# Kernel optimization log

Hardware: AMD Instinct MI355X
Metric: run time of the kernel (lower is better)

## Reference

```python
import jax, jax.numpy as jnp
import numpy as np

B, H, W, C = 64, 224, 224, 3
K = 16          # num_clusters
ITERS = 10      # num_iterations
N = H * W       # pixels per image


def _kmeans_single(x, key):
    # x: [N, D] pixels of one image
    # random shuffle -> first K rows as initial centroids (matches tf.random.shuffle + slice)
    perm = jax.random.permutation(key, N)
    cent0 = x[perm[:K]]  # [K, D]

    def step(cent, _):
        # pairwise squared distances: [K, N]
        d = jnp.sum(jnp.square(x[None, :, :] - cent[:, None, :]), axis=2)
        assign = jnp.argmin(d, axis=0)                      # [N] int
        onehot = jax.nn.one_hot(assign, K, dtype=x.dtype)   # [N, K]
        sums = onehot.T @ x                                 # [K, D]
        counts = jnp.sum(onehot, axis=0)[:, None]           # [K, 1]
        # mean of assigned pixels; empty cluster -> 0/0 = NaN, same as tf.reduce_mean of empty
        new_cent = sums / counts
        return new_cent, None

    cent, _ = jax.lax.scan(step, cent0, None, length=ITERS)
    return cent.reshape(K * C)  # tf.reshape(centroids, [dims*num_clusters]) on [K,D]


def setup_inputs() -> dict:
    key = jax.random.key(0)
    inputs = jax.random.uniform(key, (B, H, W, C), dtype=jnp.float32) * 255.0
    return {"inputs": inputs}


def reference(inputs):
    x = inputs.astype(jnp.float32).reshape(B, N, C)
    keys = jax.random.split(jax.random.key(42), B)
    return jax.vmap(_kmeans_single)(x, keys)  # [B, K*C]
```

## Files before the change

kernel.cpp:

```cpp
#include <hip/hip_runtime.h>
#include <stdint.h>


#define NB    64
#define NPIX  50176
#define NK    16
#define NCH   3
#define NITER 10
#define HBINS 2048
#define CANDCAP 1024
#define COLLCAP 128
#define NBLK  512
#define NGRP  8
#define GRPSZ (NBLK / NGRP)
#define CHUNK (NPIX / 8)
#define NQUADS (CHUNK / 4)

typedef unsigned long long u64;

struct KeyPair { uint32_t a, b; };

__device__ __forceinline__ uint32_t rotl32(uint32_t v, uint32_t r) {
  return (v << r) | (v >> (32u - r));
}
__device__ __forceinline__ void tf_round(uint32_t& x0, uint32_t& x1, uint32_t r) {
  x0 += x1; x1 = rotl32(x1, r); x1 ^= x0;
}

__device__ __forceinline__ KeyPair threefry(uint32_t k0, uint32_t k1,
                                            uint32_t x0, uint32_t x1) {
  const uint32_t ks2 = k0 ^ k1 ^ 0x1BD11BDAu;
  x0 += k0; x1 += k1;
  tf_round(x0, x1, 13u); tf_round(x0, x1, 15u); tf_round(x0, x1, 26u); tf_round(x0, x1, 6u);
  x0 += k1;  x1 += ks2 + 1u;
  tf_round(x0, x1, 17u); tf_round(x0, x1, 29u); tf_round(x0, x1, 16u); tf_round(x0, x1, 24u);
  x0 += ks2; x1 += k0 + 2u;
  tf_round(x0, x1, 13u); tf_round(x0, x1, 15u); tf_round(x0, x1, 26u); tf_round(x0, x1, 6u);
  x0 += k0;  x1 += k1 + 3u;
  tf_round(x0, x1, 17u); tf_round(x0, x1, 29u); tf_round(x0, x1, 16u); tf_round(x0, x1, 24u);
  x0 += k1;  x1 += ks2 + 4u;
  tf_round(x0, x1, 13u); tf_round(x0, x1, 15u); tf_round(x0, x1, 26u); tf_round(x0, x1, 6u);
  x0 += ks2; x1 += k0 + 5u;
  KeyPair r; r.a = x0; r.b = x1; return r;
}

__device__ __forceinline__ uint32_t sortkey(KeyPair S, uint32_t i) {
  KeyPair r = threefry(S.a, S.b, 0u, i);
  return r.a ^ r.b;
}

__device__ __forceinline__ void derive_keys(int b, KeyPair& S1, KeyPair& S2) {
  KeyPair root; root.a = 0u; root.b = 42u;
  KeyPair kb = threefry(root.a, root.b, 0u, (uint32_t)b);
  KeyPair K1 = threefry(kb.a, kb.b, 0u, 0u);
  S1 = threefry(kb.a, kb.b, 0u, 1u);
  S2 = threefry(K1.a, K1.b, 0u, 1u);
}

#define T2VAL 27394240u

__device__ __forceinline__ uint32_t ald_u32(const uint32_t* p) {
  return __hip_atomic_load(p, __ATOMIC_RELAXED, __HIP_MEMORY_SCOPE_AGENT);
}
__device__ __forceinline__ void ast_f64(double* p, double v) {
  __hip_atomic_store(p, v, __ATOMIC_RELAXED, __HIP_MEMORY_SCOPE_AGENT);
}
__device__ __forceinline__ double ald_f64(const double* p) {
  return __hip_atomic_load(p, __ATOMIC_RELAXED, __HIP_MEMORY_SCOPE_AGENT);
}


__device__ __forceinline__ void gbar_full(uint32_t* bar, int blk) {
  __syncthreads();
  if (threadIdx.x == 0) {
    uint32_t* grp  = bar + ((blk & (NGRP - 1)) << 4);
    uint32_t* root = bar + 128;
    uint32_t* gen  = bar + 144;
    uint32_t g = __hip_atomic_load(gen, __ATOMIC_RELAXED, __HIP_MEMORY_SCOPE_AGENT);
    __builtin_amdgcn_fence(__ATOMIC_RELEASE, "agent");
    uint32_t a = __hip_atomic_fetch_add(grp, 1u, __ATOMIC_RELAXED,
                                        __HIP_MEMORY_SCOPE_AGENT);
    if (a == (uint32_t)GRPSZ - 1u) {
      __hip_atomic_store(grp, 0u, __ATOMIC_RELAXED, __HIP_MEMORY_SCOPE_AGENT);
      uint32_t r = __hip_atomic_fetch_add(root, 1u, __ATOMIC_RELAXED,
                                          __HIP_MEMORY_SCOPE_AGENT);
      if (r == (uint32_t)NGRP - 1u) {
        __hip_atomic_store(root, 0u, __ATOMIC_RELAXED, __HIP_MEMORY_SCOPE_AGENT);
        __hip_atomic_store(gen, g + 1u, __ATOMIC_RELEASE, __HIP_MEMORY_SCOPE_AGENT);
      } else {
        while (__hip_atomic_load(gen, __ATOMIC_RELAXED,
                                 __HIP_MEMORY_SCOPE_AGENT) == g)
          __builtin_amdgcn_s_sleep(1);
      }
    } else {
      while (__hip_atomic_load(gen, __ATOMIC_RELAXED,
                               __HIP_MEMORY_SCOPE_AGENT) == g)
        __builtin_amdgcn_s_sleep(1);
    }
    __builtin_amdgcn_fence(__ATOMIC_ACQUIRE, "agent");
  }
  __syncthreads();
}

__device__ __forceinline__ void gbar_light(uint32_t* bar, int blk) {
  __syncthreads();
  if (threadIdx.x == 0) {
    uint32_t* grp  = bar + ((blk & (NGRP - 1)) << 4);
    uint32_t* root = bar + 128;
    uint32_t* gen  = bar + 144;
    uint32_t g = __hip_atomic_load(gen, __ATOMIC_RELAXED, __HIP_MEMORY_SCOPE_AGENT);
    uint32_t a = __hip_atomic_fetch_add(grp, 1u, __ATOMIC_RELEASE,
                                        __HIP_MEMORY_SCOPE_AGENT);
    if (a == (uint32_t)GRPSZ - 1u) {
      uint32_t r = __hip_atomic_fetch_add(root, 1u, __ATOMIC_RELEASE,
                                          __HIP_MEMORY_SCOPE_AGENT);
      if (r == (uint32_t)NGRP - 1u) {
        __hip_atomic_store(root, 0u, __ATOMIC_RELAXED, __HIP_MEMORY_SCOPE_AGENT);
        __hip_atomic_store(grp, 0u, __ATOMIC_RELAXED, __HIP_MEMORY_SCOPE_AGENT);
        __hip_atomic_fetch_add(gen, 1u, __ATOMIC_RELAXED, __HIP_MEMORY_SCOPE_AGENT);
      } else {
        __hip_atomic_store(grp, 0u, __ATOMIC_RELAXED, __HIP_MEMORY_SCOPE_AGENT);
        while (__hip_atomic_load(gen, __ATOMIC_RELAXED,
                                 __HIP_MEMORY_SCOPE_AGENT) == g)
          __builtin_amdgcn_s_sleep(1);
      }
    } else {
      while (__hip_atomic_load(gen, __ATOMIC_RELAXED,
                               __HIP_MEMORY_SCOPE_AGENT) == g)
        __builtin_amdgcn_s_sleep(1);
    }
  }
  __syncthreads();
}

union SMem {
  struct { uint32_t lh[HBINS]; } p1;
  struct { u64 sc[CANDCAP]; uint32_t sh[HBINS]; uint32_t S[HBINS];
           uint32_t ts[256]; uint32_t Rt[NK]; } p2;
  struct { uint32_t bs[NK]; } p3;
  struct { u64 lc[NK * COLLCAP]; int jsel[NK]; } p4;
  struct { float accf[64 * 256]; } p5;
};

__global__ __launch_bounds__(256, 2) void mega(
    const float* __restrict__ x, float* __restrict__ out,
    float* __restrict__ cent, double* __restrict__ sums,
    uint32_t* __restrict__ ncand, uint32_t* __restrict__ ncoll,
    uint32_t* __restrict__ bar, uint32_t* __restrict__ hist,
    uint32_t* __restrict__ binsel, uint32_t* __restrict__ rem,
    u64* __restrict__ cand, u64* __restrict__ coll) {
  __shared__ SMem sm;
  const int blk = (int)blockIdx.x;
  const int tid = (int)threadIdx.x;
  const int b = blk >> 3;
  const int c = blk & 7;

  KeyPair S1, S2;
  derive_keys(b, S1, S2);

  for (int i = tid; i < HBINS; i += 256) sm.p1.lh[i] = 0u;
  __syncthreads();
  {
    const int start = c * CHUNK;
    for (int i = start + tid; i < start + CHUNK; i += 256) {
      uint32_t k2 = sortkey(S2, (uint32_t)i);
      if (k2 < T2VAL) {
        uint32_t p = atomicAdd(&ncand[b], 1u);
        if (p < CANDCAP) cand[b * CANDCAP + p] = ((u64)k2 << 32) | (uint32_t)i;
      }
      uint32_t k1 = sortkey(S1, (uint32_t)i);
      atomicAdd(&sm.p1.lh[k1 >> 21], 1u);
    }
    __syncthreads();
    for (int i = tid; i < HBINS; i += 256)
      if (sm.p1.lh[i]) atomicAdd(&hist[b * HBINS + i], sm.p1.lh[i]);
  }
  gbar_full(bar, blk);

  if (blk < NB) {
    const int bb = blk;
    uint32_t nc = ald_u32(&ncand[bb]);
    const int M = nc < CANDCAP ? (int)nc : CANDCAP;
    for (int i = tid; i < M; i += 256) sm.p2.sc[i] = cand[bb * CANDCAP + i];
    for (int i = tid; i < HBINS; i += 256) sm.p2.sh[i] = hist[bb * HBINS + i];
    __syncthreads();
    for (int j = tid; j < M; j += 256) {
      u64 me = sm.p2.sc[j];
      int r = 0;
      for (int t = 0; t < M; ++t) r += (sm.p2.sc[t] < me) ? 1 : 0;
      if (r < NK) sm.p2.Rt[r] = (uint32_t)(me & 0xffffffffu);
    }
    uint32_t loc[8]; uint32_t run = 0;
    for (int j = 0; j < 8; ++j) { run += sm.p2.sh[tid * 8 + j]; loc[j] = run; }
    sm.p2.ts[tid] = run;
    __syncthreads();
    for (int off = 1; off < 256; off <<= 1) {
      uint32_t v = (tid >= off) ? sm.p2.ts[tid - off] : 0u;
      __syncthreads();
      sm.p2.ts[tid] += v;
      __syncthreads();
    }
    uint32_t excl = sm.p2.ts[tid] - run;
    for (int j = 0; j < 8; ++j) sm.p2.S[tid * 8 + j] = excl + loc[j];
    __syncthreads();
    if (tid < NK) {
      uint32_t R = sm.p2.Rt[tid];
      int lo = 0, hi = HBINS - 1;
      while (lo < hi) {
        int mid = (lo + hi) >> 1;
        if (sm.p2.S[mid] > R) hi = mid; else lo = mid + 1;
      }
      binsel[bb * NK + tid] = (uint32_t)lo;
      rem[bb * NK + tid] = R - (lo ? sm.p2.S[lo - 1] : 0u);
    }
  }
  gbar_full(bar, blk);

  {
    __shared__ uint32_t bs_s[NK];
    if (tid < NK) bs_s[tid] = binsel[b * NK + tid];
    __syncthreads();
    const int start = c * CHUNK;
    for (int i = start + tid; i < start + CHUNK; i += 256) {
      uint32_t k1 = sortkey(S1, (uint32_t)i);
      uint32_t pb = k1 >> 21;
      #pragma unroll
      for (int t = 0; t < NK; ++t) {
        if (pb == bs_s[t]) {
          uint32_t p = atomicAdd(&ncoll[b * NK + t], 1u);
          if (p < COLLCAP)
            coll[(b * NK + t) * COLLCAP + p] = ((u64)k1 << 32) | (uint32_t)i;
        }
      }
    }
  }
  gbar_full(bar, blk);

  if (blk < NB) {
    const int bb = blk;
    for (int i = tid; i < NK * COLLCAP; i += 256)
      sm.p4.lc[i] = coll[bb * NK * COLLCAP + i];
    __syncthreads();
    if (tid < NK) {
      uint32_t ncl = ncoll[bb * NK + tid];
      const int m = ncl < COLLCAP ? (int)ncl : COLLCAP;
      const uint32_t r = rem[bb * NK + tid];
      const u64* cc = &sm.p4.lc[tid * COLLCAP];
      u64 lo = 0ULL, cur = ~0ULL;
      bool first = true;
      for (uint32_t pass = 0; pass <= r; ++pass) {
        cur = ~0ULL;
        for (int i = 0; i < m; ++i) {
          u64 v = cc[i];
          if ((first || v > lo) && v < cur) cur = v;
        }
        lo = cur; first = false;
      }
      sm.p4.jsel[tid] = (int)(cur & 0xffffffffu);
    }
    __syncthreads();
    if (tid < NK * NCH) {
      int k = tid / NCH, ch = tid % NCH;
      cent[bb * NK * NCH + tid] =
          x[((size_t)bb * NPIX + (size_t)sm.p4.jsel[k]) * NCH + ch];
    }
  }
  gbar_full(bar, blk);

  const float4* px4 = (const float4*)(x + (size_t)b * NPIX * NCH + (size_t)c * (CHUNK * NCH));
  float* accf = sm.p5.accf;

  for (int it = 0; it < NITER; ++it) {
    if (tid < NK * NCH) {
      float v;
      if (it == 0) {
        v = cent[b * NK * NCH + tid];
      } else {
        const int k = tid / NCH, ch = tid - k * NCH;
        double* sb = &sums[((it - 1) % 3) * (NB * NK * 4) + b * NK * 4];
        double s = ald_f64(&sb[k * 4 + ch]);
        double n = ald_f64(&sb[k * 4 + 3]);
        v = (float)(s / n);
      }
      accf[tid] = v;
    }
    __syncthreads();
    float cr[NK * NCH];
    {
      const float4* cp = (const float4*)accf;
      #pragma unroll
      for (int i = 0; i < 12; ++i) {
        float4 t4 = cp[i];
        cr[4 * i + 0] = t4.x; cr[4 * i + 1] = t4.y;
        cr[4 * i + 2] = t4.z; cr[4 * i + 3] = t4.w;
      }
    }
    int kn = -1;
    #pragma unroll
    for (int k = NK - 1; k >= 0; --k) {
      float a = cr[3 * k], bb2 = cr[3 * k + 1], cc2 = cr[3 * k + 2];
      if (a != a || bb2 != bb2 || cc2 != cc2) kn = k;
    }
    __syncthreads();
    {
      float4 z4 = make_float4(0.f, 0.f, 0.f, 0.f);
      float4* zp = (float4*)accf;
      #pragma unroll
      for (int i = 0; i < 16; ++i) zp[tid + 256 * i] = z4;
      if (tid < NK * 4)
        ast_f64(&sums[((it + 1) % 3) * (NB * NK * 4) + b * NK * 4 + tid], 0.0);
    }
    __syncthreads();
    float* a0 = &accf[tid];
    for (int j = tid; j < NQUADS; j += 256) {
      const float4 A = px4[3 * j], Bv = px4[3 * j + 1], Cv = px4[3 * j + 2];
      const float qx[4][3] = {{A.x, A.y, A.z}, {A.w, Bv.x, Bv.y},
                              {Bv.z, Bv.w, Cv.x}, {Cv.y, Cv.z, Cv.w}};
      #pragma unroll
      for (int q = 0; q < 4; ++q) {
        const float v0 = qx[q][0], v1 = qx[q][1], v2 = qx[q][2];
        int best = 0;
        float bd = 3.402823466e38f;
        #pragma unroll
        for (int k = 0; k < NK; ++k) {
          float d0 = __fsub_rn(v0, cr[3 * k + 0]);
          float d1 = __fsub_rn(v1, cr[3 * k + 1]);
          float d2 = __fsub_rn(v2, cr[3 * k + 2]);
          float d = __fadd_rn(__fadd_rn(__fmul_rn(d0, d0), __fmul_rn(d1, d1)),
                              __fmul_rn(d2, d2));
          bool cnd = d < bd;
          bd = cnd ? d : bd;
          best = cnd ? k : best;
        }
        if (kn >= 0) best = kn;
        const int r = best << 10;
        a0[r]       += v0;
        a0[r + 256] += v1;
        a0[r + 512] += v2;
        a0[r + 768] += 1.0f;
      }
    }
    __syncthreads();
    double part = 0.0;
    {
      const int r = tid & 63, q = tid >> 6;
      const float4* rp = (const float4*)&accf[r * 256 + q * 64];
      const int s0 = r & 15;
      #pragma unroll
      for (int m = 0; m < 16; ++m) {
        float4 t4 = rp[(m + s0) & 15];
        part += (double)t4.x + (double)t4.y + (double)t4.z + (double)t4.w;
      }
    }
    __syncthreads();
    {
      double* red = (double*)accf;
      red[tid] = part;
      __syncthreads();
      if (tid < 64) {
        double tot = red[tid] + red[64 + tid] + red[128 + tid] + red[192 + tid];
        atomicAdd(&sums[(it % 3) * (NB * NK * 4) + b * NK * 4 + tid], tot);
      }
    }
    gbar_light(bar, blk);
  }

  if (c == 0 && tid < NK * NCH) {
    const int k = tid / NCH, ch = tid - k * NCH;
    double* sb = &sums[((NITER - 1) % 3) * (NB * NK * 4) + b * NK * 4];
    out[b * NK * NCH + tid] = (float)(ald_f64(&sb[k * 4 + ch]) /
                                      ald_f64(&sb[k * 4 + 3]));
  }
}

__global__ __launch_bounds__(256) void kinit_mono(const float* __restrict__ x,
                                                  float* __restrict__ cent,
                                                  float* __restrict__ sums) {
  const int b = (int)blockIdx.x;
  const int tid = (int)threadIdx.x;
  __shared__ u64 cand[CANDCAP];
  __shared__ u64 coll[NK][COLLCAP];
  __shared__ uint32_t hist[HBINS];
  __shared__ uint32_t Rtgt[NK];
  __shared__ uint32_t binsel[NK];
  __shared__ uint32_t rem[NK];
  __shared__ int jsel[NK];
  __shared__ int ncand;
  __shared__ int ncoll[NK];
  KeyPair S1, S2;
  derive_keys(b, S1, S2);
  if (tid == 0) ncand = 0;
  if (tid < NK) ncoll[tid] = 0;
  for (int i = tid; i < HBINS; i += 256) hist[i] = 0u;
  __syncthreads();
  for (int i = tid; i < NPIX; i += 256) {
    uint32_t k2 = sortkey(S2, (uint32_t)i);
    if (k2 < T2VAL) {
      int p = atomicAdd(&ncand, 1);
      if (p < CANDCAP) cand[p] = ((u64)k2 << 32) | (uint32_t)i;
    }
    uint32_t k1 = sortkey(S1, (uint32_t)i);
    atomicAdd(&hist[k1 >> 21], 1u);
  }
  __syncthreads();
  const int M = ncand < CANDCAP ? ncand : CANDCAP;
  for (int j = tid; j < M; j += 256) {
    u64 me = cand[j];
    int rank = 0;
    for (int t = 0; t < M; ++t) rank += (cand[t] < me) ? 1 : 0;
    if (rank < NK) Rtgt[rank] = (uint32_t)(me & 0xffffffffu);
  }
  __syncthreads();
  if (tid < NK) {
    uint32_t R = Rtgt[tid], cum = 0u, bin = 0u;
    for (int i = 0; i < HBINS; ++i) {
      uint32_t h = hist[i];
      if (R < cum + h) { bin = (uint32_t)i; break; }
      cum += h;
    }
    binsel[tid] = bin;
    rem[tid] = R - cum;
  }
  __syncthreads();
  for (int i = tid; i < NPIX; i += 256) {
    uint32_t k1 = sortkey(S1, (uint32_t)i);
    uint32_t pb = k1 >> 21;
    #pragma unroll
    for (int t = 0; t < NK; ++t) {
      if (pb == binsel[t]) {
        int p = atomicAdd(&ncoll[t], 1);
        if (p < COLLCAP) coll[t][p] = ((u64)k1 << 32) | (uint32_t)i;
      }
    }
  }
  __syncthreads();
  if (tid < NK) {
    int m = ncoll[tid] < COLLCAP ? ncoll[tid] : COLLCAP;
    uint32_t r = rem[tid];
    u64 lo = 0ULL, cur = ~0ULL;
    bool first = true;
    for (uint32_t pass = 0; pass <= r; ++pass) {
      cur = ~0ULL;
      for (int t = 0; t < m; ++t) {
        u64 v = coll[tid][t];
        if ((first || v > lo) && v < cur) cur = v;
      }
      lo = cur; first = false;
    }
    jsel[tid] = (int)(cur & 0xffffffffu);
  }
  __syncthreads();
  if (tid < NK * NCH) {
    int k = tid / NCH, c = tid % NCH;
    cent[(b * NK + k) * NCH + c] = x[((size_t)b * NPIX + (size_t)jsel[k]) * NCH + c];
  }
  if (tid < NK * 4) sums[b * NK * 4 + tid] = 0.0f;
}

__global__ __launch_bounds__(256) void kassign(const float* __restrict__ x,
                                               const float* __restrict__ cent,
                                               float* __restrict__ sums) {
  const int b = (int)blockIdx.y;
  const int tid = (int)threadIdx.x;
  __shared__ float cs[NK * NCH];
  __shared__ float acc[4][NK * 4];
  __shared__ int knan_s;
  if (tid < NK * NCH) cs[tid] = cent[b * NK * NCH + tid];
  acc[tid >> 6][tid & 63] = 0.0f;
  __syncthreads();
  if (tid == 0) {
    int kn = -1;
    for (int k = 0; k < NK; ++k) {
      float a = cs[3 * k], bb = cs[3 * k + 1], cc = cs[3 * k + 2];
      if (a != a || bb != bb || cc != cc) { kn = k; break; }
    }
    knan_s = kn;
  }
  __syncthreads();
  float cr[NK * NCH];
  #pragma unroll
  for (int i = 0; i < NK * NCH; ++i) cr[i] = cs[i];
  const float* xb = x + (size_t)b * NPIX * NCH;
  const float4* p = (const float4*)(xb + (size_t)blockIdx.x * 3072);
  const float4 A = p[3 * tid], Bv = p[3 * tid + 1], Cv = p[3 * tid + 2];
  const float px[4][3] = {{A.x, A.y, A.z}, {A.w, Bv.x, Bv.y},
                          {Bv.z, Bv.w, Cv.x}, {Cv.y, Cv.z, Cv.w}};
  float* a0 = acc[tid >> 6];
  const int kn = knan_s;
  #pragma unroll
  for (int q = 0; q < 4; ++q) {
    const float v0 = px[q][0], v1 = px[q][1], v2 = px[q][2];
    int best = 0;
    float bd = 3.402823466e38f;
    #pragma unroll
    for (int k = 0; k < NK; ++k) {
      float d0 = __fsub_rn(v0, cr[3 * k + 0]);
      float d1 = __fsub_rn(v1, cr[3 * k + 1]);
      float d2 = __fsub_rn(v2, cr[3 * k + 2]);
      float d = __fadd_rn(__fadd_rn(__fmul_rn(d0, d0), __fmul_rn(d1, d1)),
                          __fmul_rn(d2, d2));
      bool cnd = d < bd;
      bd = cnd ? d : bd;
      best = cnd ? k : best;
    }
    if (kn >= 0) best = kn;
    atomicAdd(&a0[best * 4 + 0], v0);
    atomicAdd(&a0[best * 4 + 1], v1);
    atomicAdd(&a0[best * 4 + 2], v2);
    atomicAdd(&a0[best * 4 + 3], 1.0f);
  }
  __syncthreads();
  if (tid < NK * 4) {
    float v = acc[0][tid] + acc[1][tid] + acc[2][tid] + acc[3][tid];
    atomicAdd(&sums[b * NK * 4 + tid], v);
  }
}

__global__ __launch_bounds__(64) void kupdate(float* __restrict__ cent,
                                              float* __restrict__ sums,
                                              float* __restrict__ out) {
  const int b = (int)blockIdx.x;
  const int t = (int)threadIdx.x;
  float v = 0.0f;
  if (t < NK * NCH) {
    const int k = t / NCH, c = t % NCH;
    v = sums[b * NK * 4 + k * 4 + c] / sums[b * NK * 4 + k * 4 + 3];
  }
  __syncthreads();
  if (t < NK * NCH) {
    cent[b * NK * NCH + t] = v;
    out[b * NK * NCH + t] = v;
  }
  sums[b * NK * 4 + t] = 0.0f;
}

extern "C" void kernel_launch(void* const* d_in, const int* in_sizes, int n_in,
                              void* d_out, int out_size, void* d_ws, size_t ws_size,
                              hipStream_t stream) {
  (void)in_sizes; (void)n_in; (void)out_size;
  const float* x = (const float*)d_in[0];
  float* out = (float*)d_out;
  char* ws = (char*)d_ws;

  float*    cent   = (float*)(ws + 0);
  double*   sums   = (double*)(ws + 12288);
  uint32_t* ncand  = (uint32_t*)(ws + 110592);
  uint32_t* ncoll  = (uint32_t*)(ws + 110848);
  uint32_t* bar    = (uint32_t*)(ws + 114944);
  uint32_t* hist   = (uint32_t*)(ws + 115968);
  uint32_t* binsel = (uint32_t*)(ws + 640256);
  uint32_t* rem    = (uint32_t*)(ws + 644352);
  u64*      cand   = (u64*)(ws + 648448);
  u64*      coll   = (u64*)(ws + 1172736);
  const size_t REQ = 2221312;

  if (ws_size >= REQ) {
    hipMemsetAsync(ws + 110592, 0, 529664, stream);
    mega<<<NBLK, 256, 0, stream>>>(x, out, cent, sums, ncand, ncoll, bar,
                                   hist, binsel, rem, cand, coll);
  } else {
    float* centf = (float*)ws;
    float* sumsf = centf + NB * NK * NCH;
    kinit_mono<<<NB, 256, 0, stream>>>(x, centf, sumsf);
    for (int it = 0; it < NITER; ++it) {
      kassign<<<dim3(49, NB), 256, 0, stream>>>(x, centf, sumsf);
      kupdate<<<NB, 64, 0, stream>>>(centf, sumsf, out);
    }
  }
}
```

Measured before the change: 547.8 us.

## Split each image across 16 blocks with smaller shared atomic accumulators and prefetch

Doubles the per-image block count from 8 to 16 (1024 persistent blocks, 4 per CU) by shrinking the shared accumulator from per-thread slots to per-lane slots updated with LDS atomics. It also software-prefetches the next pixel quad, and the barrier group layout and workspace offsets are adjusted to match. The aim is more occupancy and memory-latency hiding in the assignment loop. The costs are LDS atomic contention among the four wavefronts sharing each lane slot, and a grid barrier that now has to coordinate 1024 co-resident blocks, which risks deadlock if they cannot all be resident.

```diff
diff --git a/kernel.cpp b/kernel.cpp
--- a/kernel.cpp
+++ b/kernel.cpp
@@ -10,10 +10,11 @@
 #define HBINS 2048
 #define CANDCAP 1024
 #define COLLCAP 128
-#define NBLK  512
-#define NGRP  8
+#define NCHK  16
+#define NBLK  (NB * NCHK)
+#define NGRP  16
 #define GRPSZ (NBLK / NGRP)
-#define CHUNK (NPIX / 8)
+#define CHUNK (NPIX / NCHK)
 #define NQUADS (CHUNK / 4)
 
 typedef unsigned long long u64;
@@ -74,8 +75,8 @@
   __syncthreads();
   if (threadIdx.x == 0) {
     uint32_t* grp  = bar + ((blk & (NGRP - 1)) << 4);
-    uint32_t* root = bar + 128;
-    uint32_t* gen  = bar + 144;
+    uint32_t* root = bar + 256;
+    uint32_t* gen  = bar + 272;
     uint32_t g = __hip_atomic_load(gen, __ATOMIC_RELAXED, __HIP_MEMORY_SCOPE_AGENT);
     __builtin_amdgcn_fence(__ATOMIC_RELEASE, "agent");
     uint32_t a = __hip_atomic_fetch_add(grp, 1u, __ATOMIC_RELAXED,
@@ -106,8 +107,8 @@
   __syncthreads();
   if (threadIdx.x == 0) {
     uint32_t* grp  = bar + ((blk & (NGRP - 1)) << 4);
-    uint32_t* root = bar + 128;
-    uint32_t* gen  = bar + 144;
+    uint32_t* root = bar + 256;
+    uint32_t* gen  = bar + 272;
     uint32_t g = __hip_atomic_load(gen, __ATOMIC_RELAXED, __HIP_MEMORY_SCOPE_AGENT);
     uint32_t a = __hip_atomic_fetch_add(grp, 1u, __ATOMIC_RELEASE,
                                         __HIP_MEMORY_SCOPE_AGENT);
@@ -137,12 +138,11 @@
   struct { uint32_t lh[HBINS]; } p1;
   struct { u64 sc[CANDCAP]; uint32_t sh[HBINS]; uint32_t S[HBINS];
            uint32_t ts[256]; uint32_t Rt[NK]; } p2;
-  struct { uint32_t bs[NK]; } p3;
   struct { u64 lc[NK * COLLCAP]; int jsel[NK]; } p4;
-  struct { float accf[64 * 256]; } p5;
+  struct { float accf[64 * 64]; } p5;
 };
 
-__global__ __launch_bounds__(256, 2) void mega(
+__global__ __launch_bounds__(256, 4) void mega(
     const float* __restrict__ x, float* __restrict__ out,
     float* __restrict__ cent, double* __restrict__ sums,
     uint32_t* __restrict__ ncand, uint32_t* __restrict__ ncoll,
@@ -152,8 +152,8 @@
   __shared__ SMem sm;
   const int blk = (int)blockIdx.x;
   const int tid = (int)threadIdx.x;
-  const int b = blk >> 3;
-  const int c = blk & 7;
+  const int b = blk >> 4;
+  const int c = blk & (NCHK - 1);
 
   KeyPair S1, S2;
   derive_keys(b, S1, S2);
@@ -269,6 +269,7 @@
 
   const float4* px4 = (const float4*)(x + (size_t)b * NPIX * NCH + (size_t)c * (CHUNK * NCH));
   float* accf = sm.p5.accf;
+  const int lane = tid & 63;
 
   for (int it = 0; it < NITER; ++it) {
     if (tid < NK * NCH) {
@@ -306,14 +307,19 @@
       float4 z4 = make_float4(0.f, 0.f, 0.f, 0.f);
       float4* zp = (float4*)accf;
       #pragma unroll
-      for (int i = 0; i < 16; ++i) zp[tid + 256 * i] = z4;
+      for (int i = 0; i < 4; ++i) zp[tid + 256 * i] = z4;
       if (tid < NK * 4)
         ast_f64(&sums[((it + 1) % 3) * (NB * NK * 4) + b * NK * 4 + tid], 0.0);
     }
     __syncthreads();
-    float* a0 = &accf[tid];
-    for (int j = tid; j < NQUADS; j += 256) {
-      const float4 A = px4[3 * j], Bv = px4[3 * j + 1], Cv = px4[3 * j + 2];
+    float* a0 = &accf[lane];
+    int j = tid;
+    float4 A, Bv, Cv;
+    if (j < NQUADS) { A = px4[3 * j]; Bv = px4[3 * j + 1]; Cv = px4[3 * j + 2]; }
+    while (j < NQUADS) {
+      const int jn = j + 256;
+      float4 An, Bn, Cn;
+      if (jn < NQUADS) { An = px4[3 * jn]; Bn = px4[3 * jn + 1]; Cn = px4[3 * jn + 2]; }
       const float qx[4][3] = {{A.x, A.y, A.z}, {A.w, Bv.x, Bv.y},
                               {Bv.z, Bv.w, Cv.x}, {Cv.y, Cv.z, Cv.w}};
       #pragma unroll
@@ -333,24 +339,21 @@
           best = cnd ? k : best;
         }
         if (kn >= 0) best = kn;
-        const int r = best << 10;
-        a0[r]       += v0;
-        a0[r + 256] += v1;
-        a0[r + 512] += v2;
-        a0[r + 768] += 1.0f;
-      }
+        const int r = best << 8;
+        atomicAdd(&a0[r], v0);
+        atomicAdd(&a0[r + 64], v1);
+        atomicAdd(&a0[r + 128], v2);
+        atomicAdd(&a0[r + 192], 1.0f);
+      }
+      A = An; Bv = Bn; Cv = Cn; j = jn;
     }
     __syncthreads();
     double part = 0.0;
     {
       const int r = tid & 63, q = tid >> 6;
-      const float4* rp = (const float4*)&accf[r * 256 + q * 64];
-      const int s0 = r & 15;
+      const float* rp = &accf[r * 64 + q * 16];
       #pragma unroll
-      for (int m = 0; m < 16; ++m) {
-        float4 t4 = rp[(m + s0) & 15];
-        part += (double)t4.x + (double)t4.y + (double)t4.z + (double)t4.w;
-      }
+      for (int m = 0; m < 16; ++m) part += (double)rp[(m + r) & 15];
     }
     __syncthreads();
     {
@@ -547,15 +550,15 @@
   uint32_t* ncand  = (uint32_t*)(ws + 110592);
   uint32_t* ncoll  = (uint32_t*)(ws + 110848);
   uint32_t* bar    = (uint32_t*)(ws + 114944);
-  uint32_t* hist   = (uint32_t*)(ws + 115968);
-  uint32_t* binsel = (uint32_t*)(ws + 640256);
-  uint32_t* rem    = (uint32_t*)(ws + 644352);
-  u64*      cand   = (u64*)(ws + 648448);
-  u64*      coll   = (u64*)(ws + 1172736);
-  const size_t REQ = 2221312;
+  uint32_t* hist   = (uint32_t*)(ws + 116992);
+  uint32_t* binsel = (uint32_t*)(ws + 641280);
+  uint32_t* rem    = (uint32_t*)(ws + 645376);
+  u64*      cand   = (u64*)(ws + 649472);
+  u64*      coll   = (u64*)(ws + 1173760);
+  const size_t REQ = 2222336;
 
   if (ws_size >= REQ) {
-    hipMemsetAsync(ws + 110592, 0, 529664, stream);
+    hipMemsetAsync(ws + 110592, 0, 530688, stream);
     mega<<<NBLK, 256, 0, stream>>>(x, out, cent, sums, ncand, ncoll, bar,
                                    hist, binsel, rem, cand, coll);
   } else {
```

Result: slower. 1.078 ms (+96.8%).
